# Performance work log

Measured on AMD Instinct MI355X. Metric: run time of the kernel, lower is better.

The kernel has to match this reference:

```python
import jax, jax.numpy as jnp
import numpy as np

K_SIZE = 5


def extract_patches(x, k):
    # tf.image.extract_patches with SAME padding, stride 1, rate 1.
    # x: (B, H, W, C) -> (B, H, W, k*k, C), patch index ordered row-major (ki, kj),
    # channels last within each tap, matching TF's depth ordering + reshape.
    B, H, W, C = x.shape
    p = k // 2
    xp = jnp.pad(x, ((0, 0), (p, p), (p, p), (0, 0)))
    views = [xp[:, i:i + H, j:j + W, :] for i in range(k) for j in range(k)]
    return jnp.stack(views, axis=3)


def setup_inputs() -> dict:
    key = jax.random.key(0)
    k1, k2, k3, k4 = jax.random.split(key, 4)
    B, H, W, C = 4, 64, 64, 128
    bin_size = 128
    return {
        "main": jax.random.normal(k1, (B, H, W, C), dtype=jnp.float32),
        "main_value": jax.random.normal(k2, (B, H, W, bin_size), dtype=jnp.float32),
        "ref": jax.random.normal(k3, (B, H, W, C), dtype=jnp.float32),
        "ref_value": jax.random.normal(k4, (B, H, W, bin_size), dtype=jnp.float32),
    }


def reference(main, main_value, ref, ref_value):
    # mode == 'dot'
    k = K_SIZE
    main5 = main[:, :, :, None, :]                 # (B,H,W,1,C)
    main_value5 = main_value[:, :, :, None, :]     # (B,H,W,1,bin)
    ref_stacked = extract_patches(ref, k)          # (B,H,W,k*k,C)
    ref_value_stacked = extract_patches(ref_value, k)  # (B,H,W,k*k,bin)
    # concat the center query itself as an extra key/value slot
    ref_con = jnp.concatenate([ref_stacked, main5], axis=3)        # (B,H,W,k*k+1,C)
    attn = jnp.sum(ref_con * main5, axis=4)                         # (B,H,W,k*k+1)
    attn = jax.nn.softmax(attn, axis=3)
    val_con = jnp.concatenate([ref_value_stacked, main_value5], axis=3)  # (B,H,W,k*k+1,bin)
    out = jnp.sum(attn[..., None] * val_con, axis=3)                # (B,H,W,bin)
    return out
```

## Files before the change

### kernel.cpp

```cpp
#include <hip/hip_runtime.h>
#include <math.h>

typedef _Float16 v8h __attribute__((ext_vector_type(8)));
typedef float    v4f __attribute__((ext_vector_type(4)));

#define B_OFF   0
#define ALO_OFF 32768
#define L_OFF   40960
#define P_OFF   57344

__device__ __forceinline__ int swz(int r, int c16) {
    return (r << 8) + ((c16 ^ (r & 15)) << 4);
}

__global__ __launch_bounds__(512, 4) void local_attn_mfma2(
    const float* __restrict__ main_,
    const float* __restrict__ main_value,
    const float* __restrict__ ref,
    const float* __restrict__ ref_value,
    float* __restrict__ out)
{
    __shared__ __align__(16) char S[65536];

    const int tid = threadIdx.x;
    const int bid = blockIdx.x;
    const int b  = bid >> 7;
    const int h0 = ((bid >> 3) & 15) << 2;
    const int w0 = (bid & 7) << 3;
    const int lane = tid & 63, w = tid >> 6;

    const int r = tid >> 2;
    const int q = tid & 3;
    bool valid = true;
    const float* src;
    if (r < 96) {
        const int hy = r / 12, hx = r - hy * 12;
        const int gh = h0 - 2 + hy, gw = w0 - 2 + hx;
        valid = (gh >= 0) & (gh < 64) & (gw >= 0) & (gw < 64);
        src = ref + (size_t)((((b << 6) + (valid ? gh : 0)) << 6) + (valid ? gw : 0)) * 128;
    } else {
        const int t = r - 96;
        src = main_ + (size_t)((((b << 6) + h0 + (t >> 3)) << 6) + (w0 + (t & 7))) * 128;
    }
    float4 e1[8];
    #pragma unroll
    for (int g = 0; g < 8; ++g)
        e1[g] = valid ? *(const float4*)(src + (q << 5) + (g << 2)) : make_float4(0, 0, 0, 0);

    float pv[4][8];
    #pragma unroll
    for (int i = 0; i < 4; ++i) {
        const int tk = w + (i << 3);
        const int pb = tk & 15;
        const int ch = ((tk >> 4) << 6) + lane;
        #pragma unroll
        for (int j = 0; j < 8; ++j) {
            const int pos = (pb << 3) + j;
            float v = 0.f;
            if (pos < 96) {
                const int hy = pos / 12, hx = pos - hy * 12;
                const int gh = h0 - 2 + hy, gw = w0 - 2 + hx;
                if ((gh >= 0) & (gh < 64) & (gw >= 0) & (gw < 64))
                    v = ref_value[(size_t)((((b << 6) + gh) << 6) + gw) * 128 + ch];
            } else {
                const int t2 = pos - 96;
                v = main_value[(size_t)((((b << 6) + h0 + (t2 >> 3)) << 6) + (w0 + (t2 & 7))) * 128 + ch];
            }
            pv[i][j] = v;
        }
    }

    #pragma unroll
    for (int g = 0; g < 4; ++g) {
        const float4 v0 = e1[2 * g], v1 = e1[2 * g + 1];
        float a8[8] = {v0.x, v0.y, v0.z, v0.w, v1.x, v1.y, v1.z, v1.w};
        v8h hi;
        #pragma unroll
        for (int j = 0; j < 8; ++j) hi[j] = (_Float16)a8[j];
        *(v8h*)(S + B_OFF + swz(r, (q << 2) + g)) = hi;
        if (r >= 96) {
            v8h lo;
            #pragma unroll
            for (int j = 0; j < 8; ++j) lo[j] = (_Float16)(a8[j] - (float)hi[j]);
            *(v8h*)(S + ALO_OFF + swz(r - 96, (q << 2) + g)) = lo;
        }
    }
    *(uint4*)(S + P_OFF + tid * 16) = make_uint4(0, 0, 0, 0);

    v8h hv[4];
    #pragma unroll
    for (int i = 0; i < 4; ++i)
        #pragma unroll
        for (int j = 0; j < 8; ++j) hv[i][j] = (_Float16)pv[i][j];

    __syncthreads();

    const int l15 = lane & 15, quad = lane >> 4;
    const int mt  = w >> 2;
    const int ntp = (w & 3) << 1;

    {
        const int arow = 96 + (mt << 4) + l15;
        const int lrow = (mt << 4) + l15;
        const int b0r  = (ntp << 4) + l15, b1r = b0r + 16;
        v4f acc0 = {0, 0, 0, 0}, acc1 = {0, 0, 0, 0};
        #pragma unroll
        for (int ks = 0; ks < 4; ++ks) {
            const int c16 = (ks << 2) + quad;
            const v8h ahi = *(const v8h*)(S + B_OFF   + swz(arow, c16));
            const v8h alo = *(const v8h*)(S + ALO_OFF + swz(lrow, c16));
            const v8h bb0 = *(const v8h*)(S + B_OFF   + swz(b0r,  c16));
            const v8h bb1 = *(const v8h*)(S + B_OFF   + swz(b1r,  c16));
            acc0 = __builtin_amdgcn_mfma_f32_16x16x32_f16(ahi, bb0, acc0, 0, 0, 0);
            acc0 = __builtin_amdgcn_mfma_f32_16x16x32_f16(alo, bb0, acc0, 0, 0, 0);
            acc1 = __builtin_amdgcn_mfma_f32_16x16x32_f16(ahi, bb1, acc1, 0, 0, 0);
            acc1 = __builtin_amdgcn_mfma_f32_16x16x32_f16(alo, bb1, acc1, 0, 0, 0);
        }
        #pragma unroll
        for (int j = 0; j < 4; ++j) {
            const int px = (mt << 4) + (quad << 2) + j;
            *(float*)(S + L_OFF + (px << 9) + ((((ntp    ) << 4) + l15) << 2)) = acc0[j];
            *(float*)(S + L_OFF + (px << 9) + ((((ntp + 1) << 4) + l15) << 2)) = acc1[j];
        }
    }
    __syncthreads();

    {
        #pragma unroll
        for (int i = 0; i < 4; ++i) {
            const int tk = w + (i << 3);
            const int pb = tk & 15;
            const int ch = ((tk >> 4) << 6) + lane;
            *(v8h*)(S + B_OFF + swz(ch, pb)) = hv[i];
        }
        const int half = lane >> 5;
        const int l    = lane & 31;
        #pragma unroll
        for (int i = 0; i < 2; ++i) {
            const int t = (w << 2) + (i << 1) + half;
            const int ty = t >> 3, tx = t & 7;
            const bool act = l < 26;
            int col;
            if (l < 25) {
                const int dy = l / 5 - 2, dx = l % 5 - 2;
                col = (ty + dy + 2) * 12 + (tx + dx + 2);
            } else col = 96 + t;
            const float lg = act ? *(const float*)(S + L_OFF + (t << 9) + (col << 2)) : -INFINITY;
            float m = lg;
            #pragma unroll
            for (int off = 16; off; off >>= 1) m = fmaxf(m, __shfl_xor(m, off));
            const float e = act ? __expf(lg - m) : 0.f;
            float s = e;
            #pragma unroll
            for (int off = 16; off; off >>= 1) s += __shfl_xor(s, off);
            if (act)
                *(_Float16*)(S + P_OFF + swz(t, col >> 3) + ((col & 7) << 1)) = (_Float16)(e / s);
        }
    }
    __syncthreads();

    {
        const int prow = (mt << 4) + l15;
        const int v0r  = (ntp << 4) + l15, v1r = v0r + 16;
        v4f acc0 = {0, 0, 0, 0}, acc1 = {0, 0, 0, 0};
        #pragma unroll
        for (int ks = 0; ks < 4; ++ks) {
            const int c16 = (ks << 2) + quad;
            const v8h pa  = *(const v8h*)(S + P_OFF + swz(prow, c16));
            const v8h vt0 = *(const v8h*)(S + B_OFF + swz(v0r,  c16));
            const v8h vt1 = *(const v8h*)(S + B_OFF + swz(v1r,  c16));
            acc0 = __builtin_amdgcn_mfma_f32_16x16x32_f16(pa, vt0, acc0, 0, 0, 0);
            acc1 = __builtin_amdgcn_mfma_f32_16x16x32_f16(pa, vt1, acc1, 0, 0, 0);
        }
        #pragma unroll
        for (int j = 0; j < 4; ++j) {
            const int px = (mt << 4) + (quad << 2) + j;
            const size_t gbase =
                (size_t)((((b << 6) + h0 + (px >> 3)) << 6) + (w0 + (px & 7))) * 128;
            out[gbase + ((ntp    ) << 4) + l15] = acc0[j];
            out[gbase + ((ntp + 1) << 4) + l15] = acc1[j];
        }
    }
}

extern "C" void kernel_launch(void* const* d_in, const int* in_sizes, int n_in,
                              void* d_out, int out_size, void* d_ws, size_t ws_size,
                              hipStream_t stream) {
    const float* main_      = (const float*)d_in[0];
    const float* main_value = (const float*)d_in[1];
    const float* ref        = (const float*)d_in[2];
    const float* ref_value  = (const float*)d_in[3];
    float* out = (float*)d_out;

    dim3 grid(4 * 16 * 8), block(512);
    local_attn_mfma2<<<grid, block, 0, stream>>>(main_, main_value, ref, ref_value, out);
}
```

Before: 98.64 us.

## Load QK operands directly into registers and compute self-logit exactly in fp32

The QK MFMA operands (main query rows and ref halo rows) are now loaded from global memory straight into registers and converted to fp16, with no staging through LDS. This drops one barrier and the LDS traffic for Q/K. The self-logit (query dotted with itself) is computed as an exact fp32 sum of squares, which replaces the hi/lo split MFMA. The value tile is written to LDS early and the logits layout shrinks, so total LDS use falls. In exchange, ref rows are read redundantly by the two M-tile warp groups, and cross-position logits lose the lo-correction term, leaving them at plain fp16 precision.

```diff
diff --git a/kernel.cpp b/kernel.cpp
--- a/kernel.cpp
+++ b/kernel.cpp
@@ -4,23 +4,24 @@
 typedef _Float16 v8h __attribute__((ext_vector_type(8)));
 typedef float    v4f __attribute__((ext_vector_type(4)));
 
-#define B_OFF   0
-#define ALO_OFF 32768
-#define L_OFF   40960
-#define P_OFF   57344
+#define VT_OFF  0
+#define L_OFF   32768
+#define P_OFF   45568
+#define SL_OFF  53760
+#define LDS_SZ  53888
 
 __device__ __forceinline__ int swz(int r, int c16) {
     return (r << 8) + ((c16 ^ (r & 15)) << 4);
 }
 
-__global__ __launch_bounds__(512, 4) void local_attn_mfma2(
+__global__ __launch_bounds__(512, 4) void local_attn_direct(
     const float* __restrict__ main_,
     const float* __restrict__ main_value,
     const float* __restrict__ ref,
     const float* __restrict__ ref_value,
     float* __restrict__ out)
 {
-    __shared__ __align__(16) char S[65536];
+    __shared__ __align__(16) char S[LDS_SZ];
 
     const int tid = threadIdx.x;
     const int bid = blockIdx.x;
@@ -28,31 +29,17 @@
     const int h0 = ((bid >> 3) & 15) << 2;
     const int w0 = (bid & 7) << 3;
     const int lane = tid & 63, w = tid >> 6;
+    const int l15 = lane & 15, quad = lane >> 4;
+    const int mt = w >> 2, wl = w & 3;
 
-    const int r = tid >> 2;
-    const int q = tid & 3;
-    bool valid = true;
-    const float* src;
-    if (r < 96) {
-        const int hy = r / 12, hx = r - hy * 12;
-        const int gh = h0 - 2 + hy, gw = w0 - 2 + hx;
-        valid = (gh >= 0) & (gh < 64) & (gw >= 0) & (gw < 64);
-        src = ref + (size_t)((((b << 6) + (valid ? gh : 0)) << 6) + (valid ? gw : 0)) * 128;
-    } else {
-        const int t = r - 96;
-        src = main_ + (size_t)((((b << 6) + h0 + (t >> 3)) << 6) + (w0 + (t & 7))) * 128;
-    }
-    float4 e1[8];
-    #pragma unroll
-    for (int g = 0; g < 8; ++g)
-        e1[g] = valid ? *(const float4*)(src + (q << 5) + (g << 2)) : make_float4(0, 0, 0, 0);
+    *(uint4*)(S + P_OFF + tid * 16) = make_uint4(0, 0, 0, 0);
 
-    float pv[4][8];
     #pragma unroll
     for (int i = 0; i < 4; ++i) {
-        const int tk = w + (i << 3);
+        const int tk = (w << 2) + i;
         const int pb = tk & 15;
         const int ch = ((tk >> 4) << 6) + lane;
+        float pvv[8];
         #pragma unroll
         for (int j = 0; j < 8; ++j) {
             const int pos = (pb << 3) + j;
@@ -66,86 +53,85 @@
                 const int t2 = pos - 96;
                 v = main_value[(size_t)((((b << 6) + h0 + (t2 >> 3)) << 6) + (w0 + (t2 & 7))) * 128 + ch];
             }
-            pv[i][j] = v;
+            pvv[j] = v;
+        }
+        v8h hv;
+        #pragma unroll
+        for (int j = 0; j < 8; ++j) hv[j] = (_Float16)pvv[j];
+        *(v8h*)(S + VT_OFF + swz(ch, pb)) = hv;
+    }
+
+    v8h a[4];
+    float sq = 0.f;
+    {
+        const int px = (mt << 4) + l15;
+        const float* ap = main_ + (size_t)((((b << 6) + h0 + (px >> 3)) << 6) + (w0 + (px & 7))) * 128;
+        #pragma unroll
+        for (int ks = 0; ks < 4; ++ks) {
+            const float4 v0 = *(const float4*)(ap + (ks << 5) + (quad << 3));
+            const float4 v1 = *(const float4*)(ap + (ks << 5) + (quad << 3) + 4);
+            const float a8[8] = {v0.x, v0.y, v0.z, v0.w, v1.x, v1.y, v1.z, v1.w};
+            #pragma unroll
+            for (int j = 0; j < 8; ++j) {
+                a[ks][j] = (_Float16)a8[j];
+                sq += a8[j] * a8[j];
+            }
+        }
+        if (wl == 0) {
+            sq += __shfl_xor(sq, 16);
+            sq += __shfl_xor(sq, 32);
+            if (quad == 0) *(float*)(S + SL_OFF + (px << 2)) = sq;
         }
     }
-
     #pragma unroll
-    for (int g = 0; g < 4; ++g) {
-        const float4 v0 = e1[2 * g], v1 = e1[2 * g + 1];
-        float a8[8] = {v0.x, v0.y, v0.z, v0.w, v1.x, v1.y, v1.z, v1.w};
-        v8h hi;
-        #pragma unroll
-        for (int j = 0; j < 8; ++j) hi[j] = (_Float16)a8[j];
-        *(v8h*)(S + B_OFF + swz(r, (q << 2) + g)) = hi;
-        if (r >= 96) {
-            v8h lo;
+    for (int nn = 0; nn < 2; ++nn) {
+        const int nt = wl + (nn << 2);
+        if (nt < 6) {
+            const int hr = (nt << 4) + l15;
+            const int hy = hr / 12, hx = hr - hy * 12;
+            const int gh = h0 - 2 + hy, gw = w0 - 2 + hx;
+            const bool ok = (gh >= 0) & (gh < 64) & (gw >= 0) & (gw < 64);
+            const float* bp = ref + (size_t)((((b << 6) + (ok ? gh : 0)) << 6) + (ok ? gw : 0)) * 128;
+            v4f acc = {0, 0, 0, 0};
             #pragma unroll
-            for (int j = 0; j < 8; ++j) lo[j] = (_Float16)(a8[j] - (float)hi[j]);
-            *(v8h*)(S + ALO_OFF + swz(r - 96, (q << 2) + g)) = lo;
-        }
-    }
-    *(uint4*)(S + P_OFF + tid * 16) = make_uint4(0, 0, 0, 0);
-
-    v8h hv[4];
-    #pragma unroll
-    for (int i = 0; i < 4; ++i)
-        #pragma unroll
-        for (int j = 0; j < 8; ++j) hv[i][j] = (_Float16)pv[i][j];
-
-    __syncthreads();
-
-    const int l15 = lane & 15, quad = lane >> 4;
-    const int mt  = w >> 2;
-    const int ntp = (w & 3) << 1;
-
-    {
-        const int arow = 96 + (mt << 4) + l15;
-        const int lrow = (mt << 4) + l15;
-        const int b0r  = (ntp << 4) + l15, b1r = b0r + 16;
-        v4f acc0 = {0, 0, 0, 0}, acc1 = {0, 0, 0, 0};
-        #pragma unroll
-        for (int ks = 0; ks < 4; ++ks) {
-            const int c16 = (ks << 2) + quad;
-            const v8h ahi = *(const v8h*)(S + B_OFF   + swz(arow, c16));
-            const v8h alo = *(const v8h*)(S + ALO_OFF + swz(lrow, c16));
-            const v8h bb0 = *(const v8h*)(S + B_OFF   + swz(b0r,  c16));
-            const v8h bb1 = *(const v8h*)(S + B_OFF   + swz(b1r,  c16));
-            acc0 = __builtin_amdgcn_mfma_f32_16x16x32_f16(ahi, bb0, acc0, 0, 0, 0);
-            acc0 = __builtin_amdgcn_mfma_f32_16x16x32_f16(alo, bb0, acc0, 0, 0, 0);
-            acc1 = __builtin_amdgcn_mfma_f32_16x16x32_f16(ahi, bb1, acc1, 0, 0, 0);
-            acc1 = __builtin_amdgcn_mfma_f32_16x16x32_f16(alo, bb1, acc1, 0, 0, 0);
-        }
-        #pragma unroll
-        for (int j = 0; j < 4; ++j) {
-            const int px = (mt << 4) + (quad << 2) + j;
-            *(float*)(S + L_OFF + (px << 9) + ((((ntp    ) << 4) + l15) << 2)) = acc0[j];
-            *(float*)(S + L_OFF + (px << 9) + ((((ntp + 1) << 4) + l15) << 2)) = acc1[j];
+            for (int ks = 0; ks < 4; ++ks) {
+                float4 v0 = make_float4(0, 0, 0, 0), v1 = v0;
+                if (ok) {
+                    v0 = *(const float4*)(bp + (ks << 5) + (quad << 3));
+                    v1 = *(const float4*)(bp + (ks << 5) + (quad << 3) + 4);
+                }
+                const float b8[8] = {v0.x, v0.y, v0.z, v0.w, v1.x, v1.y, v1.z, v1.w};
+                v8h bh;
+                #pragma unroll
+                for (int j = 0; j < 8; ++j) bh[j] = (_Float16)b8[j];
+                acc = __builtin_amdgcn_mfma_f32_16x16x32_f16(a[ks], bh, acc, 0, 0, 0);
+            }
+            #pragma unroll
+            for (int j = 0; j < 4; ++j) {
+                const int px = (mt << 4) + (quad << 2) + j;
+                *(float*)(S + L_OFF + px * 400 + (((nt << 4) + l15) << 2)) = acc[j];
+            }
         }
     }
     __syncthreads();
 
     {
+        const int half = lane >> 5, l = lane & 31;
         #pragma unroll
-        for (int i = 0; i < 4; ++i) {
-            const int tk = w + (i << 3);
-            const int pb = tk & 15;
-            const int ch = ((tk >> 4) << 6) + lane;
-            *(v8h*)(S + B_OFF + swz(ch, pb)) = hv[i];
-        }
-        const int half = lane >> 5;
-        const int l    = lane & 31;
-        #pragma unroll
-        for (int i = 0; i < 2; ++i) {
-            const int t = (w << 2) + (i << 1) + half;
+        for (int it = 0; it < 2; ++it) {
+            const int t = (w << 2) + (it << 1) + half;
             const int ty = t >> 3, tx = t & 7;
             const bool act = l < 26;
-            int col;
+            int col = 0;
+            float lg = -INFINITY;
             if (l < 25) {
                 const int dy = l / 5 - 2, dx = l % 5 - 2;
                 col = (ty + dy + 2) * 12 + (tx + dx + 2);
-            } else col = 96 + t;
-            const float lg = act ? *(const float*)(S + L_OFF + (t << 9) + (col << 2)) : -INFINITY;
+                lg = *(const float*)(S + L_OFF + t * 400 + (col << 2));
+            } else if (l == 25) {
+                col = 96 + t;
+                lg = *(const float*)(S + SL_OFF + (t << 2));
+            }
             float m = lg;
             #pragma unroll
             for (int off = 16; off; off >>= 1) m = fmaxf(m, __shfl_xor(m, off));
@@ -160,15 +146,16 @@
     __syncthreads();
 
     {
+        const int ntp = wl << 1;
         const int prow = (mt << 4) + l15;
-        const int v0r  = (ntp << 4) + l15, v1r = v0r + 16;
+        const int v0r = (ntp << 4) + l15, v1r = v0r + 16;
         v4f acc0 = {0, 0, 0, 0}, acc1 = {0, 0, 0, 0};
         #pragma unroll
         for (int ks = 0; ks < 4; ++ks) {
             const int c16 = (ks << 2) + quad;
-            const v8h pa  = *(const v8h*)(S + P_OFF + swz(prow, c16));
-            const v8h vt0 = *(const v8h*)(S + B_OFF + swz(v0r,  c16));
-            const v8h vt1 = *(const v8h*)(S + B_OFF + swz(v1r,  c16));
+            const v8h pa  = *(const v8h*)(S + P_OFF  + swz(prow, c16));
+            const v8h vt0 = *(const v8h*)(S + VT_OFF + swz(v0r,  c16));
+            const v8h vt1 = *(const v8h*)(S + VT_OFF + swz(v1r,  c16));
             acc0 = __builtin_amdgcn_mfma_f32_16x16x32_f16(pa, vt0, acc0, 0, 0, 0);
             acc1 = __builtin_amdgcn_mfma_f32_16x16x32_f16(pa, vt1, acc1, 0, 0, 0);
         }
@@ -193,5 +180,5 @@
     float* out = (float*)d_out;
 
     dim3 grid(4 * 16 * 8), block(512);
-    local_attn_mfma2<<<grid, block, 0, stream>>>(main_, main_value, ref, ref_value, out);
+    local_attn_direct<<<grid, block, 0, stream>>>(main_, main_value, ref, ref_value, out);
 }
```

Measured after the change: 98.87 us. Within noise of the previous version (+0.2%).
